# Optimization experiments

Measured on AMD Instinct MI355X. Metric: run time of the kernel, lower is better.

Reference implementation:

```python
import jax, jax.numpy as jnp
import numpy as np

B, C, K, T = 8, 256, 64, 1000
NORM_EPS = 1e-12


def setup_inputs() -> dict:
    key = jax.random.key(0)
    k_x, k_codes, k_scales = jax.random.split(key, 3)
    init_val = 1.0 / (K * C) ** 0.5
    x = jax.random.normal(k_x, (B, C, T), dtype=jnp.float32)
    codes = jax.random.uniform(k_codes, (C, K), dtype=jnp.float32,
                               minval=-init_val, maxval=init_val)
    scales = jax.random.uniform(k_scales, (K,), dtype=jnp.float32,
                                minval=0.0, maxval=1.0)
    return {"x": x, "codes": codes, "scales": scales}


def l2_normalize(t, axis, eps=NORM_EPS):
    n = jnp.sqrt(jnp.sum(t * t, axis=axis, keepdims=True))
    n = jnp.maximum(n, eps)
    return t / n


def reference(x, codes, scales):
    # x: (B, C, T); codes: (C, K); scales: (K,)
    residual = x[:, :, None, :] - codes[None, :, :, None]      # (B, C, K, T)
    residual_l2sqr = jnp.sum(residual * residual, axis=1)      # (B, K, T)
    weights_tc = jax.nn.softmax(-scales[None, :, None] * residual_l2sqr, axis=1)  # softmax over codes K
    embeddings = jnp.einsum('bckt,bkt->bkc', residual, weights_tc) / x.shape[-1]  # (B, K, C)
    embeddings = l2_normalize(embeddings, axis=-1)
    return embeddings
```

## Files before the change

### kernel.cpp

```cpp
#include <hip/hip_runtime.h>
#include <stdint.h>

constexpr int Bn  = 8;
constexpr int Cn  = 256;
constexpr int Kn  = 64;
constexpr int Tn  = 1000;
constexpr int CH  = 16;
constexpr int NCH = 64;
constexpr int TW  = 256;
constexpr int NTQ = 4;

constexpr int XT_P = 264;
constexpr int MW_P = 20;
constexpr int XC_P = 264;

typedef float f32x4 __attribute__((ext_vector_type(4)));
typedef __bf16 bf16x8 __attribute__((ext_vector_type(8)));

__device__ __forceinline__ unsigned short f2bf(float f) {
    unsigned u = __float_as_uint(f);
    return (unsigned short)((u + 0x7FFFu + ((u >> 16) & 1u)) >> 16);
}

__global__ __launch_bounds__(256) void lde_prep(
    const float* __restrict__ codes, unsigned short* __restrict__ cT,
    float* __restrict__ csq)
{
    const int k = blockIdx.x, c = threadIdx.x;
    const int lane = c & 63, wv = c >> 6;
    float v = codes[c * Kn + k];
    cT[k * Cn + c] = f2bf(v);
    float q = v * v;
#pragma unroll
    for (int off = 32; off >= 1; off >>= 1) q += __shfl_xor(q, off, 64);
    __shared__ float red[4];
    if (lane == 0) red[wv] = q;
    __syncthreads();
    if (c == 0) csq[k] = red[0] + red[1] + red[2] + red[3];
}

__global__ __launch_bounds__(256) void lde_w(
    const float* __restrict__ x,
    const unsigned short* __restrict__ cT,
    const float* __restrict__ csq_g,
    const float* __restrict__ scales,
    unsigned short* __restrict__ w_g,
    float* __restrict__ Sp)
{
    __shared__ __align__(16) unsigned short xT[CH * XT_P];
    __shared__ float Mw[Kn * MW_P];
    __shared__ float xsqp[16 * 17];
    __shared__ float xsq[CH];
    __shared__ float spw[4 * 64];

    const int tid  = threadIdx.x;
    const int wave = tid >> 6;
    const int lane = tid & 63;
    const int n    = lane & 15;
    const int q    = lane >> 4;
    const int b    = blockIdx.x >> 6;
    const int ch   = blockIdx.x & 63;
    const int t0   = ch * CH;
    const float* xb = x + (size_t)b * Cn * Tn;

#pragma unroll
    for (int r = 0; r < 4; ++r) {
        int idx = r * 256 + tid;
        int c = idx >> 2, tf = idx & 3;
        int t = t0 + 4 * tf;
        float4 v;
        if (t + 3 < Tn) {
            v = *(const float4*)(xb + c * Tn + t);
        } else {
            v.x = (t     < Tn) ? xb[c * Tn + t]     : 0.f;
            v.y = (t + 1 < Tn) ? xb[c * Tn + t + 1] : 0.f;
            v.z = (t + 2 < Tn) ? xb[c * Tn + t + 2] : 0.f;
            v.w = (t + 3 < Tn) ? xb[c * Tn + t + 3] : 0.f;
        }
        xT[(4 * tf + 0) * XT_P + c] = f2bf(v.x);
        xT[(4 * tf + 1) * XT_P + c] = f2bf(v.y);
        xT[(4 * tf + 2) * XT_P + c] = f2bf(v.z);
        xT[(4 * tf + 3) * XT_P + c] = f2bf(v.w);
    }
    {
        int tl = tid & 15, s = tid >> 4;
        float a = 0.f;
        if (t0 + tl < Tn) {
            const float* xp = xb + (s * 16) * Tn + t0 + tl;
#pragma unroll
            for (int i = 0; i < 16; ++i) { float v = xp[i * Tn]; a = fmaf(v, v, a); }
        }
        xsqp[s * 17 + tl] = a;
    }
    __syncthreads();

    if (tid < CH) {
        float a = 0.f;
#pragma unroll
        for (int s = 0; s < 16; ++s) a += xsqp[s * 17 + tid];
        xsq[tid] = a;
    }

    {
        const unsigned short* Ab = cT + (wave * 16 + n) * Cn + q * 8;
        const unsigned short* Bb = xT + n * XT_P + q * 8;
        f32x4 acc = {0.f, 0.f, 0.f, 0.f};
#pragma unroll
        for (int c0 = 0; c0 < Cn; c0 += 32) {
            bf16x8 aF = *(const bf16x8*)(Ab + c0);
            bf16x8 bF = *(const bf16x8*)(Bb + c0);
            acc = __builtin_amdgcn_mfma_f32_16x16x32_bf16(aF, bF, acc, 0, 0, 0);
        }
#pragma unroll
        for (int r = 0; r < 4; ++r)
            Mw[(wave * 16 + q * 4 + r) * MW_P + n] = acc[r];
    }
    __syncthreads();

    {
        const float sc = scales[lane];
        const float cq = csq_g[lane];
        unsigned short wh[4];
        float sp = 0.f;
#pragma unroll
        for (int j = 0; j < 4; ++j) {
            int t = wave * 4 + j;
            float m     = Mw[lane * MW_P + t];
            float logit = -sc * (xsq[t] - 2.f * m + cq);
            float mx = logit;
#pragma unroll
            for (int off = 32; off >= 1; off >>= 1)
                mx = fmaxf(mx, __shfl_xor(mx, off, 64));
            float e = __expf(logit - mx);
            float s = e;
#pragma unroll
            for (int off = 32; off >= 1; off >>= 1)
                s += __shfl_xor(s, off, 64);
            float wv = e / s;
            if (t0 + t >= Tn) wv = 0.f;
            sp += wv;
            wh[j] = f2bf(wv);
        }
        *(ushort4*)(w_g + ((size_t)(b * NCH + ch) * Kn + lane) * CH + wave * 4) =
            make_ushort4(wh[0], wh[1], wh[2], wh[3]);
        spw[wave * 64 + lane] = sp;
    }
    __syncthreads();

    if (wave == 0) {
        float s4 = spw[lane] + spw[64 + lane] + spw[128 + lane] + spw[192 + lane];
        Sp[((size_t)b * Kn + lane) * NCH + ch] = s4;
    }
}

__global__ __launch_bounds__(256) void lde_pool(
    const float* __restrict__ x,
    const unsigned short* __restrict__ w_g,
    float* __restrict__ part)
{
    __shared__ __align__(16) unsigned short xc[16 * XC_P];

    const int tid  = threadIdx.x;
    const int wave = tid >> 6;
    const int lane = tid & 63;
    const int n    = lane & 15;
    const int q    = lane >> 4;
    const int bid  = blockIdx.x;
    const int b    = bid >> 6;
    const int ct   = (bid >> 2) & 15;
    const int tq   = bid & 3;
    const int c0   = ct * 16;
    const int tw0  = tq * TW;
    const float* xb = x + (size_t)(b * Cn + c0) * Tn;

#pragma unroll
    for (int r = 0; r < 4; ++r) {
        int idx = r * 256 + tid;
        int cl = idx >> 6, tf = idx & 63;
        int t = tw0 + 4 * tf;
        float4 v;
        if (t + 3 < Tn) {
            v = *(const float4*)(xb + cl * Tn + t);
        } else {
            v.x = (t     < Tn) ? xb[cl * Tn + t]     : 0.f;
            v.y = (t + 1 < Tn) ? xb[cl * Tn + t + 1] : 0.f;
            v.z = (t + 2 < Tn) ? xb[cl * Tn + t + 2] : 0.f;
            v.w = (t + 3 < Tn) ? xb[cl * Tn + t + 3] : 0.f;
        }
        *(ushort4*)(xc + cl * XC_P + 4 * tf) =
            make_ushort4(f2bf(v.x), f2bf(v.y), f2bf(v.z), f2bf(v.w));
    }
    __syncthreads();

    f32x4 acc = {0.f, 0.f, 0.f, 0.f};
#pragma unroll
    for (int s = 0; s < 8; ++s) {
        int tg  = tw0 + s * 32 + q * 8;
        int chh = tg >> 4;
        int tl  = tg & 15;
        bf16x8 aF = *(const bf16x8*)(w_g + ((size_t)(b * NCH + chh) * Kn + wave * 16 + n) * CH + tl);
        bf16x8 bF = *(const bf16x8*)(xc + n * XC_P + s * 32 + q * 8);
        acc = __builtin_amdgcn_mfma_f32_16x16x32_bf16(aF, bF, acc, 0, 0, 0);
    }
    float* pb = part + ((size_t)(b * NTQ + tq) * Kn + wave * 16 + q * 4) * Cn + c0 + n;
#pragma unroll
    for (int r = 0; r < 4; ++r)
        pb[(size_t)r * Cn] = acc[r];
}

__global__ __launch_bounds__(256) void lde_fin(
    const float* __restrict__ part,
    const float* __restrict__ Sp,
    const float* __restrict__ codes,
    float* __restrict__ out)
{
    const int b    = blockIdx.x >> 6;
    const int k    = blockIdx.x & 63;
    const int tid  = threadIdx.x;
    const int lane = tid & 63;
    const int wave = tid >> 6;

    __shared__ float red[4];
    __shared__ float Ss;

    if (wave == 0) {
        float s = Sp[((size_t)b * Kn + k) * NCH + lane];
#pragma unroll
        for (int off = 32; off >= 1; off >>= 1) s += __shfl_xor(s, off, 64);
        if (lane == 0) Ss = s;
    }
    __syncthreads();
    const float S = Ss;

    const int c = tid;
    const float* pb = part + (size_t)b * NTQ * Kn * Cn + k * Cn + c;
    float val = pb[0] + pb[(size_t)Kn * Cn] + pb[(size_t)2 * Kn * Cn] + pb[(size_t)3 * Kn * Cn];

    float e = (val - codes[c * Kn + k] * S) * (1.0f / (float)Tn);

    float qq = e * e;
#pragma unroll
    for (int off = 32; off >= 1; off >>= 1) qq += __shfl_xor(qq, off, 64);
    if (lane == 0) red[wave] = qq;
    __syncthreads();
    float nn = sqrtf(red[0] + red[1] + red[2] + red[3]);

    out[((size_t)b * Kn + k) * Cn + c] = e / fmaxf(nn, 1e-12f);
}

extern "C" void kernel_launch(void* const* d_in, const int* in_sizes, int n_in,
                              void* d_out, int out_size, void* d_ws, size_t ws_size,
                              hipStream_t stream) {
    const float* x      = (const float*)d_in[0];
    const float* codes  = (const float*)d_in[1];
    const float* scales = (const float*)d_in[2];
    float* out = (float*)d_out;

    char* ws = (char*)d_ws;
    float*          part = (float*)ws;
    unsigned short* w_g  = (unsigned short*)(ws + (2u << 20));
    float*          Sp   = (float*)(ws + (3u << 20));
    unsigned short* cT   = (unsigned short*)(ws + (3u << 20) + (256u << 10));
    float*          csq  = (float*)(ws + (3u << 20) + (292u << 10));

    lde_prep<<<Kn,            256, 0, stream>>>(codes, cT, csq);
    lde_w   <<<Bn * NCH,      256, 0, stream>>>(x, cT, csq, scales, w_g, Sp);
    lde_pool<<<Bn * 16 * NTQ, 256, 0, stream>>>(x, w_g, part);
    lde_fin <<<Bn * Kn,       256, 0, stream>>>(part, Sp, codes, out);
}
```

Before: 77.63 us.

## Fuse four kernels into one cooperative kernel with grid syncs

Merges the prep, weight, pool and finalize kernels into a single cooperative launch of 512 blocks, using grid.sync between phases instead of separate kernel launches. The codes transpose, bf16 conversion and squared norms are now computed inline from the fp32 codes in each block, so the prep kernel is gone. The x squared norms are accumulated from the same float4 loads used for the transpose rather than a second pass over x. This removes launch gaps and redundant reads, but it adds grid-wide barrier cost and requires all 512 blocks to be co-resident.

```diff
diff --git a/kernel.cpp b/kernel.cpp
--- a/kernel.cpp
+++ b/kernel.cpp
@@ -1,5 +1,8 @@
 #include <hip/hip_runtime.h>
+#include <hip/hip_cooperative_groups.h>
 #include <stdint.h>
+
+namespace cg = cooperative_groups;
 
 constexpr int Bn  = 8;
 constexpr int Cn  = 256;
@@ -22,143 +25,26 @@
     return (unsigned short)((u + 0x7FFFu + ((u >> 16) & 1u)) >> 16);
 }
 
-__global__ __launch_bounds__(256) void lde_prep(
-    const float* __restrict__ codes, unsigned short* __restrict__ cT,
-    float* __restrict__ csq)
-{
-    const int k = blockIdx.x, c = threadIdx.x;
-    const int lane = c & 63, wv = c >> 6;
-    float v = codes[c * Kn + k];
-    cT[k * Cn + c] = f2bf(v);
-    float q = v * v;
-#pragma unroll
-    for (int off = 32; off >= 1; off >>= 1) q += __shfl_xor(q, off, 64);
-    __shared__ float red[4];
-    if (lane == 0) red[wv] = q;
-    __syncthreads();
-    if (c == 0) csq[k] = red[0] + red[1] + red[2] + red[3];
-}
-
-__global__ __launch_bounds__(256) void lde_w(
+union BF8 { unsigned short u[8]; bf16x8 v; };
+
+__global__ __launch_bounds__(256) void lde_all(
     const float* __restrict__ x,
-    const unsigned short* __restrict__ cT,
-    const float* __restrict__ csq_g,
+    const float* __restrict__ codes,
     const float* __restrict__ scales,
     unsigned short* __restrict__ w_g,
-    float* __restrict__ Sp)
+    float* __restrict__ Sp,
+    float* __restrict__ part,
+    float* __restrict__ out)
 {
     __shared__ __align__(16) unsigned short xT[CH * XT_P];
+    __shared__ __align__(16) unsigned short xc[16 * XC_P];
     __shared__ float Mw[Kn * MW_P];
-    __shared__ float xsqp[16 * 17];
+    __shared__ float xsqp[64 * 17];
     __shared__ float xsq[CH];
+    __shared__ float csqs[Kn];
     __shared__ float spw[4 * 64];
-
-    const int tid  = threadIdx.x;
-    const int wave = tid >> 6;
-    const int lane = tid & 63;
-    const int n    = lane & 15;
-    const int q    = lane >> 4;
-    const int b    = blockIdx.x >> 6;
-    const int ch   = blockIdx.x & 63;
-    const int t0   = ch * CH;
-    const float* xb = x + (size_t)b * Cn * Tn;
-
-#pragma unroll
-    for (int r = 0; r < 4; ++r) {
-        int idx = r * 256 + tid;
-        int c = idx >> 2, tf = idx & 3;
-        int t = t0 + 4 * tf;
-        float4 v;
-        if (t + 3 < Tn) {
-            v = *(const float4*)(xb + c * Tn + t);
-        } else {
-            v.x = (t     < Tn) ? xb[c * Tn + t]     : 0.f;
-            v.y = (t + 1 < Tn) ? xb[c * Tn + t + 1] : 0.f;
-            v.z = (t + 2 < Tn) ? xb[c * Tn + t + 2] : 0.f;
-            v.w = (t + 3 < Tn) ? xb[c * Tn + t + 3] : 0.f;
-        }
-        xT[(4 * tf + 0) * XT_P + c] = f2bf(v.x);
-        xT[(4 * tf + 1) * XT_P + c] = f2bf(v.y);
-        xT[(4 * tf + 2) * XT_P + c] = f2bf(v.z);
-        xT[(4 * tf + 3) * XT_P + c] = f2bf(v.w);
-    }
-    {
-        int tl = tid & 15, s = tid >> 4;
-        float a = 0.f;
-        if (t0 + tl < Tn) {
-            const float* xp = xb + (s * 16) * Tn + t0 + tl;
-#pragma unroll
-            for (int i = 0; i < 16; ++i) { float v = xp[i * Tn]; a = fmaf(v, v, a); }
-        }
-        xsqp[s * 17 + tl] = a;
-    }
-    __syncthreads();
-
-    if (tid < CH) {
-        float a = 0.f;
-#pragma unroll
-        for (int s = 0; s < 16; ++s) a += xsqp[s * 17 + tid];
-        xsq[tid] = a;
-    }
-
-    {
-        const unsigned short* Ab = cT + (wave * 16 + n) * Cn + q * 8;
-        const unsigned short* Bb = xT + n * XT_P + q * 8;
-        f32x4 acc = {0.f, 0.f, 0.f, 0.f};
-#pragma unroll
-        for (int c0 = 0; c0 < Cn; c0 += 32) {
-            bf16x8 aF = *(const bf16x8*)(Ab + c0);
-            bf16x8 bF = *(const bf16x8*)(Bb + c0);
-            acc = __builtin_amdgcn_mfma_f32_16x16x32_bf16(aF, bF, acc, 0, 0, 0);
-        }
-#pragma unroll
-        for (int r = 0; r < 4; ++r)
-            Mw[(wave * 16 + q * 4 + r) * MW_P + n] = acc[r];
-    }
-    __syncthreads();
-
-    {
-        const float sc = scales[lane];
-        const float cq = csq_g[lane];
-        unsigned short wh[4];
-        float sp = 0.f;
-#pragma unroll
-        for (int j = 0; j < 4; ++j) {
-            int t = wave * 4 + j;
-            float m     = Mw[lane * MW_P + t];
-            float logit = -sc * (xsq[t] - 2.f * m + cq);
-            float mx = logit;
-#pragma unroll
-            for (int off = 32; off >= 1; off >>= 1)
-                mx = fmaxf(mx, __shfl_xor(mx, off, 64));
-            float e = __expf(logit - mx);
-            float s = e;
-#pragma unroll
-            for (int off = 32; off >= 1; off >>= 1)
-                s += __shfl_xor(s, off, 64);
-            float wv = e / s;
-            if (t0 + t >= Tn) wv = 0.f;
-            sp += wv;
-            wh[j] = f2bf(wv);
-        }
-        *(ushort4*)(w_g + ((size_t)(b * NCH + ch) * Kn + lane) * CH + wave * 4) =
-            make_ushort4(wh[0], wh[1], wh[2], wh[3]);
-        spw[wave * 64 + lane] = sp;
-    }
-    __syncthreads();
-
-    if (wave == 0) {
-        float s4 = spw[lane] + spw[64 + lane] + spw[128 + lane] + spw[192 + lane];
-        Sp[((size_t)b * Kn + lane) * NCH + ch] = s4;
-    }
-}
-
-__global__ __launch_bounds__(256) void lde_pool(
-    const float* __restrict__ x,
-    const unsigned short* __restrict__ w_g,
-    float* __restrict__ part)
-{
-    __shared__ __align__(16) unsigned short xc[16 * XC_P];
+    __shared__ float red[4];
+    __shared__ float Ss;
 
     const int tid  = threadIdx.x;
     const int wave = tid >> 6;
@@ -166,86 +52,187 @@
     const int n    = lane & 15;
     const int q    = lane >> 4;
     const int bid  = blockIdx.x;
-    const int b    = bid >> 6;
-    const int ct   = (bid >> 2) & 15;
-    const int tq   = bid & 3;
-    const int c0   = ct * 16;
-    const int tw0  = tq * TW;
-    const float* xb = x + (size_t)(b * Cn + c0) * Tn;
-
-#pragma unroll
-    for (int r = 0; r < 4; ++r) {
-        int idx = r * 256 + tid;
-        int cl = idx >> 6, tf = idx & 63;
-        int t = tw0 + 4 * tf;
-        float4 v;
-        if (t + 3 < Tn) {
-            v = *(const float4*)(xb + cl * Tn + t);
-        } else {
-            v.x = (t     < Tn) ? xb[cl * Tn + t]     : 0.f;
-            v.y = (t + 1 < Tn) ? xb[cl * Tn + t + 1] : 0.f;
-            v.z = (t + 2 < Tn) ? xb[cl * Tn + t + 2] : 0.f;
-            v.w = (t + 3 < Tn) ? xb[cl * Tn + t + 3] : 0.f;
-        }
-        *(ushort4*)(xc + cl * XC_P + 4 * tf) =
-            make_ushort4(f2bf(v.x), f2bf(v.y), f2bf(v.z), f2bf(v.w));
+    cg::grid_group grid = cg::this_grid();
+
+    {
+        const int b  = bid >> 6;
+        const int ch = bid & 63;
+        const int t0 = ch * CH;
+        const float* xb = x + (size_t)b * Cn * Tn;
+
+        {
+            const int tf = tid & 3;
+            float sq0 = 0.f, sq1 = 0.f, sq2 = 0.f, sq3 = 0.f;
+#pragma unroll
+            for (int r = 0; r < 4; ++r) {
+                int c = (tid >> 2) + 64 * r;
+                int t = t0 + 4 * tf;
+                float4 v;
+                if (t + 3 < Tn) {
+                    v = *(const float4*)(xb + c * Tn + t);
+                } else {
+                    v.x = (t     < Tn) ? xb[c * Tn + t]     : 0.f;
+                    v.y = (t + 1 < Tn) ? xb[c * Tn + t + 1] : 0.f;
+                    v.z = (t + 2 < Tn) ? xb[c * Tn + t + 2] : 0.f;
+                    v.w = (t + 3 < Tn) ? xb[c * Tn + t + 3] : 0.f;
+                }
+                xT[(4 * tf + 0) * XT_P + c] = f2bf(v.x);
+                xT[(4 * tf + 1) * XT_P + c] = f2bf(v.y);
+                xT[(4 * tf + 2) * XT_P + c] = f2bf(v.z);
+                xT[(4 * tf + 3) * XT_P + c] = f2bf(v.w);
+                sq0 = fmaf(v.x, v.x, sq0);
+                sq1 = fmaf(v.y, v.y, sq1);
+                sq2 = fmaf(v.z, v.z, sq2);
+                sq3 = fmaf(v.w, v.w, sq3);
+            }
+            float* xp = xsqp + (tid >> 2) * 17 + 4 * tf;
+            xp[0] = sq0; xp[1] = sq1; xp[2] = sq2; xp[3] = sq3;
+        }
+        __syncthreads();
+
+        if (tid < CH) {
+            float a = 0.f;
+#pragma unroll
+            for (int i = 0; i < 64; ++i) a += xsqp[i * 17 + tid];
+            xsq[tid] = a;
+        }
+
+        {
+            const int kglob = wave * 16 + n;
+            const float* cod = codes + (q * 8) * Kn + kglob;
+            float csq_part = 0.f;
+            f32x4 acc = {0.f, 0.f, 0.f, 0.f};
+#pragma unroll
+            for (int c0 = 0; c0 < Cn; c0 += 32) {
+                float cf[8];
+#pragma unroll
+                for (int j = 0; j < 8; ++j) cf[j] = cod[(size_t)(c0 + j) * Kn];
+                BF8 aF;
+#pragma unroll
+                for (int j = 0; j < 8; ++j) {
+                    csq_part = fmaf(cf[j], cf[j], csq_part);
+                    aF.u[j] = f2bf(cf[j]);
+                }
+                bf16x8 bF = *(const bf16x8*)(xT + n * XT_P + c0 + q * 8);
+                acc = __builtin_amdgcn_mfma_f32_16x16x32_bf16(aF.v, bF, acc, 0, 0, 0);
+            }
+            csq_part += __shfl_xor(csq_part, 16, 64);
+            csq_part += __shfl_xor(csq_part, 32, 64);
+            if (q == 0) csqs[kglob] = csq_part;
+#pragma unroll
+            for (int r = 0; r < 4; ++r)
+                Mw[(wave * 16 + q * 4 + r) * MW_P + n] = acc[r];
+        }
+        __syncthreads();
+
+        {
+            const float sc = scales[lane];
+            const float cq = csqs[lane];
+            unsigned short wh[4];
+            float sp = 0.f;
+#pragma unroll
+            for (int j = 0; j < 4; ++j) {
+                int t = wave * 4 + j;
+                float m     = Mw[lane * MW_P + t];
+                float logit = -sc * (xsq[t] - 2.f * m + cq);
+                float mx = logit;
+#pragma unroll
+                for (int off = 32; off >= 1; off >>= 1)
+                    mx = fmaxf(mx, __shfl_xor(mx, off, 64));
+                float e = __expf(logit - mx);
+                float s = e;
+#pragma unroll
+                for (int off = 32; off >= 1; off >>= 1)
+                    s += __shfl_xor(s, off, 64);
+                float wv = e / s;
+                if (t0 + t >= Tn) wv = 0.f;
+                sp += wv;
+                wh[j] = f2bf(wv);
+            }
+            *(ushort4*)(w_g + ((size_t)(b * NCH + ch) * Kn + lane) * CH + wave * 4) =
+                make_ushort4(wh[0], wh[1], wh[2], wh[3]);
+            spw[wave * 64 + lane] = sp;
+        }
+        __syncthreads();
+        if (wave == 0) {
+            float s4 = spw[lane] + spw[64 + lane] + spw[128 + lane] + spw[192 + lane];
+            Sp[((size_t)b * Kn + lane) * NCH + ch] = s4;
+        }
     }
-    __syncthreads();
-
-    f32x4 acc = {0.f, 0.f, 0.f, 0.f};
-#pragma unroll
-    for (int s = 0; s < 8; ++s) {
-        int tg  = tw0 + s * 32 + q * 8;
-        int chh = tg >> 4;
-        int tl  = tg & 15;
-        bf16x8 aF = *(const bf16x8*)(w_g + ((size_t)(b * NCH + chh) * Kn + wave * 16 + n) * CH + tl);
-        bf16x8 bF = *(const bf16x8*)(xc + n * XC_P + s * 32 + q * 8);
-        acc = __builtin_amdgcn_mfma_f32_16x16x32_bf16(aF, bF, acc, 0, 0, 0);
+    grid.sync();
+
+    {
+        const int b   = bid >> 6;
+        const int ct  = (bid >> 2) & 15;
+        const int tq  = bid & 3;
+        const int c0  = ct * 16;
+        const int tw0 = tq * TW;
+        const float* xb = x + (size_t)(b * Cn + c0) * Tn;
+
+#pragma unroll
+        for (int r = 0; r < 4; ++r) {
+            int idx = r * 256 + tid;
+            int cl = idx >> 6, tf = idx & 63;
+            int t = tw0 + 4 * tf;
+            float4 v;
+            if (t + 3 < Tn) {
+                v = *(const float4*)(xb + cl * Tn + t);
+            } else {
+                v.x = (t     < Tn) ? xb[cl * Tn + t]     : 0.f;
+                v.y = (t + 1 < Tn) ? xb[cl * Tn + t + 1] : 0.f;
+                v.z = (t + 2 < Tn) ? xb[cl * Tn + t + 2] : 0.f;
+                v.w = (t + 3 < Tn) ? xb[cl * Tn + t + 3] : 0.f;
+            }
+            *(ushort4*)(xc + cl * XC_P + 4 * tf) =
+                make_ushort4(f2bf(v.x), f2bf(v.y), f2bf(v.z), f2bf(v.w));
+        }
+        __syncthreads();
+
+        f32x4 acc = {0.f, 0.f, 0.f, 0.f};
+#pragma unroll
+        for (int s = 0; s < 8; ++s) {
+            int tg  = tw0 + s * 32 + q * 8;
+            int chh = tg >> 4;
+            int tl  = tg & 15;
+            bf16x8 aF = *(const bf16x8*)(w_g + ((size_t)(b * NCH + chh) * Kn + wave * 16 + n) * CH + tl);
+            bf16x8 bF = *(const bf16x8*)(xc + n * XC_P + s * 32 + q * 8);
+            acc = __builtin_amdgcn_mfma_f32_16x16x32_bf16(aF, bF, acc, 0, 0, 0);
+        }
+        float* pb = part + ((size_t)(b * NTQ + tq) * Kn + wave * 16 + q * 4) * Cn + c0 + n;
+#pragma unroll
+        for (int r = 0; r < 4; ++r)
+            pb[(size_t)r * Cn] = acc[r];
     }
-    float* pb = part + ((size_t)(b * NTQ + tq) * Kn + wave * 16 + q * 4) * Cn + c0 + n;
-#pragma unroll
-    for (int r = 0; r < 4; ++r)
-        pb[(size_t)r * Cn] = acc[r];
-}
-
-__global__ __launch_bounds__(256) void lde_fin(
-    const float* __restrict__ part,
-    const float* __restrict__ Sp,
-    const float* __restrict__ codes,
-    float* __restrict__ out)
-{
-    const int b    = blockIdx.x >> 6;
-    const int k    = blockIdx.x & 63;
-    const int tid  = threadIdx.x;
-    const int lane = tid & 63;
-    const int wave = tid >> 6;
-
-    __shared__ float red[4];
-    __shared__ float Ss;
-
-    if (wave == 0) {
-        float s = Sp[((size_t)b * Kn + k) * NCH + lane];
-#pragma unroll
-        for (int off = 32; off >= 1; off >>= 1) s += __shfl_xor(s, off, 64);
-        if (lane == 0) Ss = s;
+    grid.sync();
+
+    {
+        const int b = bid >> 6;
+        const int k = bid & 63;
+
+        if (wave == 0) {
+            float s = Sp[((size_t)b * Kn + k) * NCH + lane];
+#pragma unroll
+            for (int off = 32; off >= 1; off >>= 1) s += __shfl_xor(s, off, 64);
+            if (lane == 0) Ss = s;
+        }
+        __syncthreads();
+        const float S = Ss;
+
+        const int c = tid;
+        const float* pb = part + (size_t)b * NTQ * Kn * Cn + k * Cn + c;
+        float val = pb[0] + pb[(size_t)Kn * Cn] + pb[(size_t)2 * Kn * Cn] + pb[(size_t)3 * Kn * Cn];
+
+        float e = (val - codes[c * Kn + k] * S) * (1.0f / (float)Tn);
+
+        float qq = e * e;
+#pragma unroll
+        for (int off = 32; off >= 1; off >>= 1) qq += __shfl_xor(qq, off, 64);
+        if (lane == 0) red[wave] = qq;
+        __syncthreads();
+        float nn = sqrtf(red[0] + red[1] + red[2] + red[3]);
+
+        out[((size_t)b * Kn + k) * Cn + c] = e / fmaxf(nn, 1e-12f);
     }
-    __syncthreads();
-    const float S = Ss;
-
-    const int c = tid;
-    const float* pb = part + (size_t)b * NTQ * Kn * Cn + k * Cn + c;
-    float val = pb[0] + pb[(size_t)Kn * Cn] + pb[(size_t)2 * Kn * Cn] + pb[(size_t)3 * Kn * Cn];
-
-    float e = (val - codes[c * Kn + k] * S) * (1.0f / (float)Tn);
-
-    float qq = e * e;
-#pragma unroll
-    for (int off = 32; off >= 1; off >>= 1) qq += __shfl_xor(qq, off, 64);
-    if (lane == 0) red[wave] = qq;
-    __syncthreads();
-    float nn = sqrtf(red[0] + red[1] + red[2] + red[3]);
-
-    out[((size_t)b * Kn + k) * Cn + c] = e / fmaxf(nn, 1e-12f);
 }
 
 extern "C" void kernel_launch(void* const* d_in, const int* in_sizes, int n_in,
@@ -260,11 +247,9 @@
     float*          part = (float*)ws;
     unsigned short* w_g  = (unsigned short*)(ws + (2u << 20));
     float*          Sp   = (float*)(ws + (3u << 20));
-    unsigned short* cT   = (unsigned short*)(ws + (3u << 20) + (256u << 10));
-    float*          csq  = (float*)(ws + (3u << 20) + (292u << 10));
-
-    lde_prep<<<Kn,            256, 0, stream>>>(codes, cT, csq);
-    lde_w   <<<Bn * NCH,      256, 0, stream>>>(x, cT, csq, scales, w_g, Sp);
-    lde_pool<<<Bn * 16 * NTQ, 256, 0, stream>>>(x, w_g, part);
-    lde_fin <<<Bn * Kn,       256, 0, stream>>>(part, Sp, codes, out);
+
+    void* args[] = { (void*)&x, (void*)&codes, (void*)&scales,
+                     (void*)&w_g, (void*)&Sp, (void*)&part, (void*)&out };
+    hipLaunchCooperativeKernel((const void*)lde_all, dim3(Bn * NCH), dim3(256),
+                               args, 0, stream);
 }
```

Result: slower. 189.4 us (+144.0%).
